# Performance work log

Hardware: AMD Instinct MI355X
Metric: run time of the kernel (lower is better)

The kernel has to match this reference:

```python
import jax, jax.numpy as jnp
import numpy as np

O, T = 2000, 6000
DIN, DW, DG, H = 2048, 300, 512, 512
VO, VR, L_EXTRA = 1000, 500, 4


def _mlp2(x, Wa, ba, Wb, bb):
    # two-layer MLP with ReLU after every Linear (sg2im build_mlp, final_nonlinearity=True)
    return jax.nn.relu(jax.nn.relu(x @ Wa + ba) @ Wb + bb)


def _triple_conv(obj_vecs, pred_vecs, s, o, Wa, ba, Wb, bb, W2a, b2a, W2b, b2b, alpha=1.0):
    # gather-by-edge -> edge MLP -> scatter-avg back to nodes (GraphTripleConv, pooling='avg')
    n_obj = obj_vecs.shape[0]
    dout = W2b.shape[1]
    cur = jnp.concatenate([obj_vecs[s], pred_vecs, obj_vecs[o]], axis=1)  # [T, 2*Din+Dp]
    t = _mlp2(cur, Wa, ba, Wb, bb)                                        # [T, 2H+Dout]
    new_s, new_p, new_o = t[:, :H], t[:, H:H + dout], t[:, H + dout:]
    pooled = jnp.zeros((n_obj, H), t.dtype).at[s].add(new_s).at[o].add(new_o)
    cnt = jnp.zeros((n_obj,), t.dtype).at[s].add(1.0).at[o].add(1.0)
    pooled = pooled / jnp.maximum(cnt, 1.0)[:, None]
    new_obj = alpha * _mlp2(pooled, W2a, b2a, W2b, b2b)
    return new_obj, new_p


def setup_inputs() -> dict:
    key = jax.random.key(0)
    ks = jax.random.split(key, 32)
    w = lambda k, sh: (jax.random.normal(k, sh, jnp.float32) * 0.02)
    inp = {
        'obj_embs': jax.random.normal(ks[0], (O, DIN), jnp.float32),
        'obj_nums': O,
        'pred_embs': jax.random.normal(ks[1], (T, DIN), jnp.float32),
        'pred_nums': T,
        'rels': jax.random.randint(ks[2], (T, 3), 0, VR, jnp.int64 if jax.config.read('jax_enable_x64') else jnp.int32),
        'objs': jax.random.randint(ks[3], (O,), 0, VO, jnp.int64 if jax.config.read('jax_enable_x64') else jnp.int32),
        # embedding tables
        'obj_table': jax.random.uniform(ks[4], (VO, DW), jnp.float32, -0.1, 0.1),
        'rel_table': jax.random.uniform(ks[5], (VR, DW), jnp.float32, -0.1, 0.1),
        # fusion layers: Linear(img_dim+word_dim -> img_dim) + relu
        'Wf_obj': w(ks[6], (DIN + DW, DIN)), 'bf_obj': jnp.zeros((DIN,), jnp.float32),
        'Wf_rel': w(ks[7], (DIN + DW, DIN)), 'bf_rel': jnp.zeros((DIN,), jnp.float32),
        # GraphTripleConv layer 1: net1 [3*DIN -> H -> 2H+DG], net2 [H -> H -> DG]
        'W1a': w(ks[8], (3 * DIN, H)), 'b1a': jnp.zeros((H,), jnp.float32),
        'W1b': w(ks[9], (H, 2 * H + DG)), 'b1b': jnp.zeros((2 * H + DG,), jnp.float32),
        'W2a': w(ks[10], (H, H)), 'b2a': jnp.zeros((H,), jnp.float32),
        'W2b': w(ks[11], (H, DG)), 'b2b': jnp.zeros((DG,), jnp.float32),
        # GraphTripleConvNet: 4 more layers, net1 [3*DG -> H -> 2H+DG], net2 [H -> H -> DG]
        'Ws1a': w(ks[12], (L_EXTRA, 3 * DG, H)), 'bs1a': jnp.zeros((L_EXTRA, H), jnp.float32),
        'Ws1b': w(ks[13], (L_EXTRA, H, 2 * H + DG)), 'bs1b': jnp.zeros((L_EXTRA, 2 * H + DG), jnp.float32),
        'Ws2a': w(ks[14], (L_EXTRA, H, H)), 'bs2a': jnp.zeros((L_EXTRA, H), jnp.float32),
        'Ws2b': w(ks[15], (L_EXTRA, H, DG)), 'bs2b': jnp.zeros((L_EXTRA, DG), jnp.float32),
    }
    return inp


def reference(obj_embs, obj_nums, pred_embs, pred_nums, rels, objs,
              obj_table, rel_table, Wf_obj, bf_obj, Wf_rel, bf_rel,
              W1a, b1a, W1b, b1b, W2a, b2a, W2b, b2b,
              Ws1a, bs1a, Ws1b, bs1b, Ws2a, bs2a, Ws2b, bs2b):
    s, p, o = rels[:, 0], rels[:, 1], rels[:, 2]
    # embedding lookup + concatenate-fusion (FusionLayer with relu)
    obj_vecs = jax.nn.relu(jnp.concatenate([obj_embs, obj_table[objs]], axis=1) @ Wf_obj + bf_obj)
    pred_vecs = jax.nn.relu(jnp.concatenate([pred_embs, rel_table[p]], axis=1) @ Wf_rel + bf_rel)
    # first GraphTripleConv (img_dim -> gconv_dim)
    obj_vecs, pred_vecs = _triple_conv(obj_vecs, pred_vecs, s, o,
                                       W1a, b1a, W1b, b1b, W2a, b2a, W2b, b2b)
    # GraphTripleConvNet: 4 more layers (gconv_dim -> gconv_dim)
    for i in range(L_EXTRA):
        obj_vecs, pred_vecs = _triple_conv(obj_vecs, pred_vecs, s, o,
                                           Ws1a[i], bs1a[i], Ws1b[i], bs1b[i],
                                           Ws2a[i], bs2a[i], Ws2b[i], bs2b[i])
    # no_imgnorm=True -> no final l2norm
    return obj_vecs, pred_vecs
```

## Files before the change

kernel.cpp:

```cpp
#include <hip/hip_runtime.h>

#define O_N 2000
#define T_N 6000
#define DIN 2048
#define DW  300
#define DG  512
#define HH_ 512

typedef __attribute__((ext_vector_type(8)))  short short8;
typedef __attribute__((ext_vector_type(16))) float f32x16;
typedef unsigned short u16;

__device__ __forceinline__ float4 ld4(const float* p) { return *(const float4*)p; }

__device__ __forceinline__ u16 rbf(float x) {
    unsigned int u = __float_as_uint(x);
    u += 0x7FFFu + ((u >> 16) & 1u);
    return (u16)(u >> 16);
}
__device__ __forceinline__ float fbf(u16 h) {
    return __uint_as_float((unsigned int)h << 16);
}
__device__ __forceinline__ void split3(float x, short& h, short& m, short& l) {
    u16 a = rbf(x);
    float r = x - fbf(a);
    u16 b = rbf(r);
    r -= fbf(b);
    u16 c = rbf(r);
    h = (short)a; m = (short)b; l = (short)c;
}

__device__ __forceinline__ void gl_lds16(u16* lds, const u16* g) {
    auto* gp = (const __attribute__((address_space(1))) unsigned int*)g;
    auto* lp = (__attribute__((address_space(3))) unsigned int*)lds;
    __builtin_amdgcn_global_load_lds(gp, lp, 16, 0, 0);
}

template<int BM, int BN, int KS>
__global__ __launch_bounds__(KS ? 512 : 256, KS ? 2 : (BM == 64 ? 4 : 2))
void gemm_mx(
    const u16* __restrict__ Ap, int MpA,
    const u16* __restrict__ Bp, int N, int KC, int M,
    const float* __restrict__ bias, int doRelu,
    float* __restrict__ C, int ldc,
    u16* __restrict__ Op, int MpO,
    const u16* __restrict__ Bp2, float* __restrict__ C2, u16* __restrict__ Op2,
    int nbx)
{
    static_assert(BM == 128 || BM == 64, "BM in {64,128}");
    constexpr int WM = BM / 2, WN = BN / 2;
    constexpr int FI = WM / 32, FJ = WN / 32;
    static_assert(!KS || FI == 2, "KS path needs FI=2");
    constexpr int UA = 6 * BM;
    constexpr int UB = 6 * BN;
    constexpr int NI = (UA + UB) / 64;
    constexpr int II = (NI + 3) / 4;
    constexpr int BUF = (BM + BN) * 48;
    __shared__ u16 sm[(KS ? 4 : 2) * BUF];

    const int tid = threadIdx.x;
    const int w = tid >> 6, lane = tid & 63;
    const int wg = w & 3;
    const int g = KS ? (w >> 2) : 0;
    const int ln31 = lane & 31, lq = lane >> 5;

    int bx = blockIdx.x;
    const u16* Bpl = Bp; float* Cl = C; u16* Opl = Op;
    if (bx >= nbx) { bx -= nbx; Bpl = Bp2; Cl = C2; Opl = Op2; }
    const int n0 = bx * BN, m0 = blockIdx.y * BM;
    const long psA = (long)KC * MpA * 8;
    const long psB = (long)KC * N * 8;

    int c0 = 0, cn = KC;
    if (KS) { int h = (KC >> 2) << 1; c0 = g ? h : 0; cn = g ? (KC - h) : h; }
    const u16* ApG = Ap + (long)c0 * MpA * 8;
    const u16* BpG = Bpl + (long)c0 * N * 8;
    u16* smg = sm + g * 2 * BUF;

    const u16* gb[II]; int gstep[II]; int lob[II]; bool gv[II];
#pragma unroll
    for (int ii = 0; ii < II; ii++) {
        int n = wg + 4 * ii;
        gv[ii] = n < NI;
        int nn = gv[ii] ? n : 0;
        int u0 = nn * 64;
        bool isA = u0 < UA;
        int uu = isA ? u0 : u0 - UA;
        int dim = isA ? BM : BN;
        int row0 = uu % dim, pq = uu / dim;
        int q = pq & 1, p = pq >> 1;
        const u16* pb = (isA ? ApG : BpG) + (long)p * (isA ? psA : psB);
        int mp = isA ? MpA : N;
        gb[ii] = pb + ((long)q * mp + (isA ? m0 : n0) + row0 + lane) * 8;
        gstep[ii] = mp * 16;
        lob[ii] = (isA ? (pq * BM + row0) : (6 * BM + pq * BN + row0)) * 8;
    }

    f32x16 ah[FI][FJ], al[FI][FJ];
#pragma unroll
    for (int fi = 0; fi < FI; fi++)
#pragma unroll
        for (int fj = 0; fj < FJ; fj++)
#pragma unroll
            for (int r = 0; r < 16; r++) { ah[fi][fj][r] = 0.f; al[fi][fj][r] = 0.f; }

    const int T = cn >> 1;
#pragma unroll
    for (int ii = 0; ii < II; ii++)
        if (gv[ii]) gl_lds16(smg + lob[ii], gb[ii]);
    __syncthreads();

    for (int t = 0; t < T; t++) {
        const int cb = (t & 1) * BUF, nb2 = ((t + 1) & 1) * BUF;
        if (t + 1 < T) {
#pragma unroll
            for (int ii = 0; ii < II; ii++)
                if (gv[ii]) gl_lds16(smg + nb2 + lob[ii],
                                     gb[ii] + (long)(t + 1) * gstep[ii]);
        }
        const u16* ab = smg + cb;
        const u16* bb = ab + 6 * BM * 8;
        short8 af[FI][3];
#pragma unroll
        for (int fi = 0; fi < FI; fi++)
#pragma unroll
            for (int p = 0; p < 3; p++)
                af[fi][p] = *(const short8*)(ab + ((p * 2 + lq) * BM + (wg >> 1) * WM + fi * 32 + ln31) * 8);
#pragma unroll
        for (int fj = 0; fj < FJ; fj++) {
            const int rB = (wg & 1) * WN + fj * 32 + ln31;
            short8 bh = *(const short8*)(bb + ((0 * 2 + lq) * BN + rB) * 8);
            short8 bm_ = *(const short8*)(bb + ((1 * 2 + lq) * BN + rB) * 8);
            short8 bl = *(const short8*)(bb + ((2 * 2 + lq) * BN + rB) * 8);
#pragma unroll
            for (int fi = 0; fi < FI; fi++) {
                ah[fi][fj] = __builtin_amdgcn_mfma_f32_32x32x16_bf16(af[fi][0], bh,  ah[fi][fj], 0, 0, 0);
                al[fi][fj] = __builtin_amdgcn_mfma_f32_32x32x16_bf16(af[fi][0], bm_, al[fi][fj], 0, 0, 0);
                al[fi][fj] = __builtin_amdgcn_mfma_f32_32x32x16_bf16(af[fi][1], bh,  al[fi][fj], 0, 0, 0);
                al[fi][fj] = __builtin_amdgcn_mfma_f32_32x32x16_bf16(af[fi][0], bl,  al[fi][fj], 0, 0, 0);
                al[fi][fj] = __builtin_amdgcn_mfma_f32_32x32x16_bf16(af[fi][1], bm_, al[fi][fj], 0, 0, 0);
                al[fi][fj] = __builtin_amdgcn_mfma_f32_32x32x16_bf16(af[fi][2], bh,  al[fi][fj], 0, 0, 0);
            }
        }
        __syncthreads();
    }

    float tv[FJ][16];
    if (KS) {
        constexpr int XW = FJ * 16 * 64;
        float* xs = (float*)sm;
        float* wrp = xs + (1 - g) * 4 * XW + wg * XW;
        if (g == 0) {
#pragma unroll
            for (int fj = 0; fj < FJ; fj++)
#pragma unroll
                for (int r = 0; r < 16; r++)
                    wrp[(fj * 16 + r) * 64 + lane] = ah[1][fj][r] + al[1][fj][r];
        } else {
#pragma unroll
            for (int fj = 0; fj < FJ; fj++)
#pragma unroll
                for (int r = 0; r < 16; r++)
                    wrp[(fj * 16 + r) * 64 + lane] = ah[0][fj][r] + al[0][fj][r];
        }
        __syncthreads();
        float* rdp = xs + g * 4 * XW + wg * XW;
        if (g == 0) {
#pragma unroll
            for (int fj = 0; fj < FJ; fj++)
#pragma unroll
                for (int r = 0; r < 16; r++)
                    tv[fj][r] = ah[0][fj][r] + al[0][fj][r] + rdp[(fj * 16 + r) * 64 + lane];
        } else {
#pragma unroll
            for (int fj = 0; fj < FJ; fj++)
#pragma unroll
                for (int r = 0; r < 16; r++)
                    tv[fj][r] = ah[1][fj][r] + al[1][fj][r] + rdp[(fj * 16 + r) * 64 + lane];
        }
        __syncthreads();
    }

    float* bounce = (float*)sm + w * 1184;
    const long psO = (long)N * MpO;
#pragma unroll
    for (int fi = 0; fi < FI; fi++) {
        if (KS && fi != g) continue;
#pragma unroll
        for (int fj = 0; fj < FJ; fj++) {
            const int colBase = n0 + (wg & 1) * WN + fj * 32;
            const int rowBase = m0 + (wg >> 1) * WM + fi * 32;
            float bv = bias ? bias[colBase + ln31] : 0.f;
            float v[16];
#pragma unroll
            for (int r = 0; r < 16; r++) {
                float s = KS ? tv[fj][r] : (ah[fi][fj][r] + al[fi][fj][r]);
                float x = s + bv;
                if (doRelu) x = fmaxf(x, 0.f);
                v[r] = x;
            }
            if (Cl) {
#pragma unroll
                for (int r = 0; r < 16; r++) {
                    int row = rowBase + (r & 3) + 8 * (r >> 2) + 4 * lq;
                    if (row < M)
                        Cl[(long)row * ldc + colBase + ln31] = v[r];
                }
            }
            if (Opl) {
#pragma unroll
                for (int r = 0; r < 16; r++)
                    bounce[((r & 3) + 8 * (r >> 2) + 4 * lq) * 36 + ln31] = v[r];
#pragma unroll
                for (int u = 0; u < 2; u++) {
                    int urow = ln31, uc = lq + 2 * u;
                    const float* rp = bounce + urow * 36 + uc * 8;
                    short8 h8, m8, l8;
#pragma unroll
                    for (int j = 0; j < 8; j++) {
                        short a, b, c2; split3(rp[j], a, b, c2);
                        h8[j] = a; m8[j] = b; l8[j] = c2;
                    }
                    long cIdx = (long)((colBase + uc * 8) >> 3);
                    long base = (cIdx * MpO + rowBase + urow) * 8;
                    *(short8*)(Opl + base) = h8;
                    *(short8*)(Opl + psO + base) = m8;
                    *(short8*)(Opl + 2 * psO + base) = l8;
                }
            }
        }
    }
}

__global__ __launch_bounds__(256) void split_b(
    const float* __restrict__ W, int K, int N, int KC,
    u16* __restrict__ Op)
{
    __shared__ float tl[64][65];
    const int tid = threadIdx.x;
    const int n0 = blockIdx.x * 64, k0 = blockIdx.y * 64;
    const long ps = (long)KC * N * 8;
#pragma unroll
    for (int l = 0; l < 4; l++) {
        int k = (tid >> 4) + l * 16;
        int nn = (tid & 15) << 2;
        float4 v = make_float4(0.f, 0.f, 0.f, 0.f);
        if (k0 + k < K) v = ld4(W + (long)(k0 + k) * N + n0 + nn);
        tl[k][nn] = v.x; tl[k][nn + 1] = v.y; tl[k][nn + 2] = v.z; tl[k][nn + 3] = v.w;
    }
    __syncthreads();
#pragma unroll
    for (int l = 0; l < 2; l++) {
        int u = tid + l * 256;
        int n = u & 63, c = u >> 6;
        short8 h8, m8, l8;
#pragma unroll
        for (int j = 0; j < 8; j++) {
            short a, b, c2; split3(tl[c * 8 + j][n], a, b, c2);
            h8[j] = a; m8[j] = b; l8[j] = c2;
        }
        long base = ((long)(k0 / 8 + c) * N + n0 + n) * 8;
        *(short8*)(Op + base) = h8;
        *(short8*)(Op + ps + base) = m8;
        *(short8*)(Op + 2 * ps + base) = l8;
    }
}

__device__ __forceinline__ void store_planes(u16* Op, long ps, long base, const float* x)
{
    short8 h8, m8, l8;
#pragma unroll
    for (int j = 0; j < 8; j++) {
        short a, b, c2; split3(x[j], a, b, c2);
        h8[j] = a; m8[j] = b; l8[j] = c2;
    }
    *(short8*)(Op + base) = h8;
    *(short8*)(Op + ps + base) = m8;
    *(short8*)(Op + 2 * ps + base) = l8;
}

__global__ __launch_bounds__(256) void split_concat_a(
    const float* __restrict__ E, int ldE, int KA,
    const float* __restrict__ Tab, int DWc,
    const int* __restrict__ idx, int idxStride,
    int mBase, int Mvalid, int Mp, int KC,
    u16* __restrict__ Op)
{
    int m = blockIdx.x * 256 + threadIdx.x;
    if (m >= Mp) return;
    int c = blockIdx.y;
    int gm = mBase + m;
    float x[8];
    if (gm >= Mvalid) {
#pragma unroll
        for (int j = 0; j < 8; j++) x[j] = 0.f;
    } else {
        int k0 = c * 8;
        if (k0 + 8 <= KA) {
            float4 a = ld4(E + (long)gm * ldE + k0);
            float4 b = ld4(E + (long)gm * ldE + k0 + 4);
            x[0] = a.x; x[1] = a.y; x[2] = a.z; x[3] = a.w;
            x[4] = b.x; x[5] = b.y; x[6] = b.z; x[7] = b.w;
        } else {
            const float* tr = Tab + (long)idx[(long)gm * idxStride] * DWc;
#pragma unroll
            for (int j = 0; j < 8; j++) {
                int k = k0 + j;
                x[j] = (k < KA) ? E[(long)gm * ldE + k]
                                : ((k - KA) < DWc ? tr[k - KA] : 0.f);
            }
        }
    }
    store_planes(Op, (long)KC * Mp * 8, ((long)c * Mp + m) * 8, x);
}

__global__ __launch_bounds__(256) void edge_planes(
    const float* __restrict__ PPv, const float* __restrict__ P1v,
    const float* __restrict__ P2v, const int* __restrict__ rels,
    const float* __restrict__ b1a, int Mp, u16* __restrict__ Op)
{
    int m = blockIdx.x * 256 + threadIdx.x;
    if (m >= Mp) return;
    int c = blockIdx.y;
    float x[8];
    if (m >= T_N) {
#pragma unroll
        for (int j = 0; j < 8; j++) x[j] = 0.f;
    } else {
        int s = rels[3 * m], o = rels[3 * m + 2];
        const float* pp = PPv + (long)m * HH_ + c * 8;
        const float* p1 = P1v + (long)s * HH_ + c * 8;
        const float* p2 = P2v + (long)o * HH_ + c * 8;
        const float* bb = b1a + c * 8;
#pragma unroll
        for (int j = 0; j < 8; j++)
            x[j] = fmaxf(pp[j] + p1[j] + p2[j] + bb[j], 0.f);
    }
    store_planes(Op, (long)64 * Mp * 8, ((long)c * Mp + m) * 8, x);
}

__global__ __launch_bounds__(256) void pool_planes(
    const float* __restrict__ PO, const int* __restrict__ CNT,
    int Mp, u16* __restrict__ Op)
{
    int m = blockIdx.x * 256 + threadIdx.x;
    if (m >= Mp) return;
    int c = blockIdx.y;
    float x[8];
    if (m >= O_N) {
#pragma unroll
        for (int j = 0; j < 8; j++) x[j] = 0.f;
    } else {
        int cc = CNT[m]; float cf = 1.f / (float)(cc < 1 ? 1 : cc);
#pragma unroll
        for (int j = 0; j < 8; j++) x[j] = PO[(long)m * HH_ + c * 8 + j] * cf;
    }
    store_planes(Op, (long)64 * Mp * 8, ((long)c * Mp + m) * 8, x);
}

__global__ __launch_bounds__(256) void predcopy_planes(
    const float* __restrict__ T2, int Mp, u16* __restrict__ Op)
{
    int m = blockIdx.x * 256 + threadIdx.x;
    if (m >= Mp) return;
    int c = blockIdx.y;
    float x[8];
    if (m >= T_N) {
#pragma unroll
        for (int j = 0; j < 8; j++) x[j] = 0.f;
    } else {
#pragma unroll
        for (int j = 0; j < 8; j++) x[j] = T2[(long)m * 1536 + 512 + c * 8 + j];
    }
    store_planes(Op, (long)64 * Mp * 8, ((long)c * Mp + m) * 8, x);
}

__global__ void predcopy_f32(const float* __restrict__ T2, float* __restrict__ dst)
{
    int i = blockIdx.x * 256 + threadIdx.x;
    if (i >= T_N * HH_ / 4) return;
    int e = i / (HH_ / 4);
    int j = (i % (HH_ / 4)) << 2;
    float4 v = ld4(T2 + (long)e * 1536 + 512 + j);
    *(float4*)(dst + (long)e * HH_ + j) = v;
}

__global__ void count_edges(const int* __restrict__ rels, int* __restrict__ CNT)
{
    int e = blockIdx.x * 256 + threadIdx.x;
    if (e >= T_N) return;
    atomicAdd(CNT + rels[3 * e + 0], 1);
    atomicAdd(CNT + rels[3 * e + 2], 1);
}

__global__ void scatter_pool(const float* __restrict__ T2,
                             const int* __restrict__ rels,
                             float* __restrict__ PO)
{
    int e = blockIdx.x;
    int t = threadIdx.x;
    int s = rels[e * 3 + 0];
    int o = rels[e * 3 + 2];
#pragma unroll
    for (int u = 0; u < 2; u++) {
        int j = t + u * 256;
        unsafeAtomicAdd(PO + (long)s * HH_ + j, T2[(long)e * 1536 + j]);
        unsafeAtomicAdd(PO + (long)o * HH_ + j, T2[(long)e * 1536 + 1024 + j]);
    }
}

template<int BM, int BN>
static inline void GX(hipStream_t st, const u16* Ap, int MpA,
                      const u16* Bp, int N, int KC, int M,
                      const float* bias, int relu_,
                      float* C, int ldc, u16* Op, int MpO,
                      const u16* Bp2, float* C2, u16* Op2)
{
    int nbx = N / BN;
    int pair = (Bp2 != nullptr) ? 2 : 1;
    dim3 g(nbx * pair, MpA / BM), b(256);
    gemm_mx<BM, BN, 0><<<g, b, 0, st>>>(Ap, MpA, Bp, N, KC, M, bias, relu_,
                                        C, ldc, Op, MpO, Bp2, C2, Op2, nbx);
}

template<int BM, int BN>
static inline void GK2(hipStream_t st, const u16* Ap, int MpA,
                       const u16* Bp, int N, int KC, int M,
                       const float* bias, int relu_,
                       float* C, int ldc, u16* Op, int MpO)
{
    dim3 g(N / BN, MpA / BM), b(512);
    gemm_mx<BM, BN, 1><<<g, b, 0, st>>>(Ap, MpA, Bp, N, KC, M, bias, relu_,
                                        C, ldc, Op, MpO,
                                        nullptr, nullptr, nullptr, N / BN);
}

static inline void SB(hipStream_t st, const float* W, int K, int N, int KC, u16* Op)
{
    dim3 g(N / 64, KC / 8), b(256);
    split_b<<<g, b, 0, st>>>(W, K, N, KC, Op);
}

extern "C" void kernel_launch(void* const* d_in, const int* in_sizes, int n_in,
                              void* d_out, int out_size, void* d_ws, size_t ws_size,
                              hipStream_t stream)
{
    const float* obj_embs  = (const float*)d_in[0];
    const float* pred_embs = (const float*)d_in[2];
    const int*   rels      = (const int*)d_in[4];
    const int*   objs      = (const int*)d_in[5];
    const float* obj_table = (const float*)d_in[6];
    const float* rel_table = (const float*)d_in[7];
    const float* Wf_obj = (const float*)d_in[8];
    const float* bf_obj = (const float*)d_in[9];
    const float* Wf_rel = (const float*)d_in[10];
    const float* bf_rel = (const float*)d_in[11];
    const float* W1a = (const float*)d_in[12];
    const float* b1a = (const float*)d_in[13];
    const float* W1b = (const float*)d_in[14];
    const float* b1b = (const float*)d_in[15];
    const float* W2a = (const float*)d_in[16];
    const float* b2a = (const float*)d_in[17];
    const float* W2b = (const float*)d_in[18];
    const float* b2b = (const float*)d_in[19];
    const float* Ws1a = (const float*)d_in[20];
    const float* bs1a = (const float*)d_in[21];
    const float* Ws1b = (const float*)d_in[22];
    const float* bs1b = (const float*)d_in[23];
    const float* Ws2a = (const float*)d_in[24];
    const float* bs2a = (const float*)d_in[25];
    const float* Ws2b = (const float*)d_in[26];
    const float* bs2b = (const float*)d_in[27];
    float* out = (float*)d_out;

    unsigned char* B8 = (unsigned char*)d_ws;
    constexpr size_t S1O  = 0;
    constexpr size_t S2O  = 29097984;
    constexpr size_t S3AO = 54263808;
    constexpr size_t ZSZ  = 86507520;
    constexpr size_t T2O  = 0;
    constexpr size_t TTO  = 36864000;
    constexpr size_t PVO  = 55345152;
    constexpr size_t PLO  = 73826304;
    constexpr size_t OVO  = 80117760;
    constexpr size_t S3BO = ZSZ;
    constexpr size_t S3CO = S3BO + 6291456;
    constexpr size_t PPO  = S3CO + 6291456;
    constexpr size_t P1O  = PPO + 12288000;
    constexpr size_t P2O  = P1O + 4096000;
    constexpr size_t CNO  = P2O + 4096000;

    u16* S1  = (u16*)(B8 + S1O);
    u16* S2  = (u16*)(B8 + S2O);
    u16* S3A = (u16*)(B8 + S3AO);
    u16* S3B = (u16*)(B8 + S3BO);
    u16* S3C = (u16*)(B8 + S3CO);
    float* T2 = (float*)(B8 + T2O);
    u16* TTp  = (u16*)(B8 + TTO);
    u16* Hp   = (u16*)(B8 + TTO);
    u16* PVp  = (u16*)(B8 + PVO);
    u16* PLp  = (u16*)(B8 + PLO);
    u16* OVp  = (u16*)(B8 + OVO);
    float* PP = (float*)(B8 + PPO);
    float* P1 = (float*)(B8 + P1O);
    float* P2 = (float*)(B8 + P2O);
    float* PO = P1;
    int* CNT  = (int*)(B8 + CNO);

    hipMemsetAsync(CNT, 0, O_N * sizeof(int), stream);
    hipLaunchKernelGGL(count_edges, dim3((T_N + 255) / 256), dim3(256), 0, stream, rels, CNT);

    SB(stream, Wf_obj, DIN + DW, DIN, 296, S3A);
    {
        dim3 g(8, 296), b(256);
        split_concat_a<<<g, b, 0, stream>>>(obj_embs, DIN, DIN, obj_table, DW,
                                            objs, 1, 0, O_N, 2048, 296, S1);
    }
    GK2<128, 128>(stream, S1, 2048, S3A, DIN, 296, O_N, bf_obj, 1,
                  nullptr, 0, S2, 2048);
    SB(stream, W1a, DIN, HH_, 256, S3B);
    SB(stream, W1a + (size_t)2 * DIN * HH_, DIN, HH_, 256, S3C);
    GX<64, 64>(stream, S2, 2048, S3B, HH_, 256, O_N, nullptr, 0,
               P1, HH_, nullptr, 0, S3C, P2, nullptr);
    SB(stream, Wf_rel, DIN + DW, DIN, 296, S3A);
    SB(stream, W1a + (size_t)DIN * HH_, DIN, HH_, 256, S3B);
    for (int ch = 0; ch < 3; ch++) {
        int ch0 = ch * 2048;
        int mp  = (ch == 2) ? 1920 : 2048;
        int mv  = (ch == 2) ? 1904 : 2048;
        dim3 g((mp + 255) / 256, 296), b(256);
        split_concat_a<<<g, b, 0, stream>>>(pred_embs, DIN, DIN, rel_table, DW,
                                            rels + 1, 3, ch0, T_N, mp, 296, S1);
        GK2<128, 128>(stream, S1, mp, S3A, DIN, 296, mv, bf_rel, 1,
                      nullptr, 0, S2, mp);
        GX<64, 64>(stream, S2, mp, S3B, HH_, 256, mv, nullptr, 0,
                   PP + (size_t)ch0 * HH_, HH_, nullptr, 0,
                   nullptr, nullptr, nullptr);
    }

    for (int L = 0; L < 5; L++) {
        const float* bb1a = (L == 0) ? b1a : (bs1a + (size_t)(L - 1) * HH_);
        const float* w1b  = (L == 0) ? W1b : (Ws1b + (size_t)(L - 1) * HH_ * 1536);
        const float* bb1b = (L == 0) ? b1b : (bs1b + (size_t)(L - 1) * 1536);
        const float* w2a  = (L == 0) ? W2a : (Ws2a + (size_t)(L - 1) * HH_ * HH_);
        const float* bb2a = (L == 0) ? b2a : (bs2a + (size_t)(L - 1) * HH_);
        const float* w2b  = (L == 0) ? W2b : (Ws2b + (size_t)(L - 1) * HH_ * DG);
        const float* bb2b = (L == 0) ? b2b : (bs2b + (size_t)(L - 1) * DG);

        if (L > 0) {
            const float* w1a = Ws1a + (size_t)(L - 1) * 3 * HH_ * HH_;
            SB(stream, w1a, HH_, HH_, 64, S3B);
            SB(stream, w1a + (size_t)2 * HH_ * HH_, HH_, HH_, 64, S3C);
            GX<64, 64>(stream, OVp, 2048, S3B, HH_, 64, O_N, nullptr, 0,
                       P1, HH_, nullptr, 0, S3C, P2, nullptr);
            SB(stream, w1a + (size_t)HH_ * HH_, HH_, HH_, 64, S3B);
            GX<64, 64>(stream, PVp, 6016, S3B, HH_, 64, T_N, nullptr, 0,
                       PP, HH_, nullptr, 0, nullptr, nullptr, nullptr);
        }

        {
            dim3 g(24, 64), b(256);
            edge_planes<<<g, b, 0, stream>>>(PP, P1, P2, rels, bb1a, 6016, TTp);
        }
        SB(stream, w1b, HH_, 1536, 64, S3C);
        GX<128, 128>(stream, TTp, 6016, S3C, 1536, 64, T_N, bb1b, 1,
                     T2, 1536, nullptr, 0, nullptr, nullptr, nullptr);
        hipMemsetAsync(PO, 0, (size_t)O_N * HH_ * sizeof(float), stream);
        hipLaunchKernelGGL(scatter_pool, dim3(T_N), dim3(256), 0, stream, T2, rels, PO);
        {
            dim3 g(8, 64), b(256);
            pool_planes<<<g, b, 0, stream>>>(PO, CNT, 2048, PLp);
        }
        SB(stream, w2a, HH_, HH_, 64, S3B);
        GX<64, 64>(stream, PLp, 2048, S3B, HH_, 64, O_N, bb2a, 1,
                   nullptr, 0, Hp, 2048, nullptr, nullptr, nullptr);
        SB(stream, w2b, HH_, DG, 64, S3C);
        if (L < 4) {
            GX<64, 64>(stream, Hp, 2048, S3C, DG, 64, O_N, bb2b, 1,
                       nullptr, 0, OVp, 2048, nullptr, nullptr, nullptr);
            dim3 g(24, 64), b(256);
            predcopy_planes<<<g, b, 0, stream>>>(T2, 6016, PVp);
        } else {
            GX<64, 64>(stream, Hp, 2048, S3C, DG, 64, O_N, bb2b, 1,
                       out, DG, nullptr, 0, nullptr, nullptr, nullptr);
            hipLaunchKernelGGL(predcopy_f32, dim3((T_N * HH_ / 4 + 255) / 256),
                               dim3(256), 0, stream, T2, out + (size_t)O_N * DG);
        }
    }
}
```

Measured before the change: 2.011 ms.

## Triple-buffer GEMM LDS tiles with prefetch depth two and explicit vmcnt waits

Moves the split-bf16 MFMA GEMM main loop from double to triple buffering in LDS, issuing global-to-LDS loads two k-steps ahead. Explicit s_waitcnt vmcnt counts with raw s_barrier replace __syncthreads, so only the oldest stage's loads are awaited. All fragments are read from LDS before a second barrier and the MFMAs run afterwards, which lets the buffer be refilled while compute proceeds. The cost is 1.5x LDS per block, which may lower occupancy. The hand-computed vmcnt values rely on every wave issuing exactly LDMIN loads per stage, which could break if the per-wave load count differs.

```diff
diff --git a/kernel.cpp b/kernel.cpp
--- a/kernel.cpp
+++ b/kernel.cpp
@@ -55,8 +55,9 @@
     constexpr int UB = 6 * BN;
     constexpr int NI = (UA + UB) / 64;
     constexpr int II = (NI + 3) / 4;
+    constexpr int LDMIN = NI / 4;
     constexpr int BUF = (BM + BN) * 48;
-    __shared__ u16 sm[(KS ? 4 : 2) * BUF];
+    __shared__ u16 sm[(KS ? 6 : 3) * BUF];
 
     const int tid = threadIdx.x;
     const int w = tid >> 6, lane = tid & 63;
@@ -75,7 +76,7 @@
     if (KS) { int h = (KC >> 2) << 1; c0 = g ? h : 0; cn = g ? (KC - h) : h; }
     const u16* ApG = Ap + (long)c0 * MpA * 8;
     const u16* BpG = Bpl + (long)c0 * N * 8;
-    u16* smg = sm + g * 2 * BUF;
+    u16* smg = sm + g * 3 * BUF;
 
     const u16* gb[II]; int gstep[II]; int lob[II]; bool gv[II];
 #pragma unroll
@@ -107,20 +108,33 @@
     const int T = cn >> 1;
 #pragma unroll
     for (int ii = 0; ii < II; ii++)
-        if (gv[ii]) gl_lds16(smg + lob[ii], gb[ii]);
-    __syncthreads();
-
+        if (gv[ii]) { gl_lds16(smg + lob[ii], gb[ii]); }
+    if (T > 1) {
+#pragma unroll
+        for (int ii = 0; ii < II; ii++)
+            if (gv[ii]) gl_lds16(smg + BUF + lob[ii], gb[ii] + (long)gstep[ii]);
+    }
+#pragma unroll
+    for (int ii = 0; ii < II; ii++) gb[ii] += (long)2 * gstep[ii];
+
+    int cb = 0, sb = 2 * BUF;
     for (int t = 0; t < T; t++) {
-        const int cb = (t & 1) * BUF, nb2 = ((t + 1) & 1) * BUF;
-        if (t + 1 < T) {
+        if (t + 2 < T) {
 #pragma unroll
             for (int ii = 0; ii < II; ii++)
-                if (gv[ii]) gl_lds16(smg + nb2 + lob[ii],
-                                     gb[ii] + (long)(t + 1) * gstep[ii]);
-        }
+                if (gv[ii]) gl_lds16(smg + sb + lob[ii], gb[ii]);
+#pragma unroll
+            for (int ii = 0; ii < II; ii++) gb[ii] += (long)gstep[ii];
+        }
+        if (t + 2 < T)      asm volatile("s_waitcnt vmcnt(%0)" :: "i"(2 * LDMIN) : "memory");
+        else if (t + 1 < T) asm volatile("s_waitcnt vmcnt(%0)" :: "i"(LDMIN) : "memory");
+        else                asm volatile("s_waitcnt vmcnt(0)" ::: "memory");
+        __builtin_amdgcn_s_barrier();
+        asm volatile("" ::: "memory");
+
         const u16* ab = smg + cb;
         const u16* bb = ab + 6 * BM * 8;
-        short8 af[FI][3];
+        short8 af[FI][3], bf[FJ][3];
 #pragma unroll
         for (int fi = 0; fi < FI; fi++)
 #pragma unroll
@@ -129,20 +143,28 @@
 #pragma unroll
         for (int fj = 0; fj < FJ; fj++) {
             const int rB = (wg & 1) * WN + fj * 32 + ln31;
-            short8 bh = *(const short8*)(bb + ((0 * 2 + lq) * BN + rB) * 8);
-            short8 bm_ = *(const short8*)(bb + ((1 * 2 + lq) * BN + rB) * 8);
-            short8 bl = *(const short8*)(bb + ((2 * 2 + lq) * BN + rB) * 8);
+#pragma unroll
+            for (int p = 0; p < 3; p++)
+                bf[fj][p] = *(const short8*)(bb + ((p * 2 + lq) * BN + rB) * 8);
+        }
+        asm volatile("s_waitcnt lgkmcnt(0)" ::: "memory");
+        __builtin_amdgcn_s_barrier();
+        asm volatile("" ::: "memory");
+
+#pragma unroll
+        for (int fj = 0; fj < FJ; fj++) {
 #pragma unroll
             for (int fi = 0; fi < FI; fi++) {
-                ah[fi][fj] = __builtin_amdgcn_mfma_f32_32x32x16_bf16(af[fi][0], bh,  ah[fi][fj], 0, 0, 0);
-                al[fi][fj] = __builtin_amdgcn_mfma_f32_32x32x16_bf16(af[fi][0], bm_, al[fi][fj], 0, 0, 0);
-                al[fi][fj] = __builtin_amdgcn_mfma_f32_32x32x16_bf16(af[fi][1], bh,  al[fi][fj], 0, 0, 0);
-                al[fi][fj] = __builtin_amdgcn_mfma_f32_32x32x16_bf16(af[fi][0], bl,  al[fi][fj], 0, 0, 0);
-                al[fi][fj] = __builtin_amdgcn_mfma_f32_32x32x16_bf16(af[fi][1], bm_, al[fi][fj], 0, 0, 0);
-                al[fi][fj] = __builtin_amdgcn_mfma_f32_32x32x16_bf16(af[fi][2], bh,  al[fi][fj], 0, 0, 0);
+                ah[fi][fj] = __builtin_amdgcn_mfma_f32_32x32x16_bf16(af[fi][0], bf[fj][0], ah[fi][fj], 0, 0, 0);
+                al[fi][fj] = __builtin_amdgcn_mfma_f32_32x32x16_bf16(af[fi][0], bf[fj][1], al[fi][fj], 0, 0, 0);
+                al[fi][fj] = __builtin_amdgcn_mfma_f32_32x32x16_bf16(af[fi][1], bf[fj][0], al[fi][fj], 0, 0, 0);
+                al[fi][fj] = __builtin_amdgcn_mfma_f32_32x32x16_bf16(af[fi][0], bf[fj][2], al[fi][fj], 0, 0, 0);
+                al[fi][fj] = __builtin_amdgcn_mfma_f32_32x32x16_bf16(af[fi][1], bf[fj][1], al[fi][fj], 0, 0, 0);
+                al[fi][fj] = __builtin_amdgcn_mfma_f32_32x32x16_bf16(af[fi][2], bf[fj][0], al[fi][fj], 0, 0, 0);
             }
         }
-        __syncthreads();
+        cb += BUF; if (cb == 3 * BUF) cb = 0;
+        sb += BUF; if (sb == 3 * BUF) sb = 0;
     }
 
     float tv[FJ][16];
```

New measurement: 1.772 ms. 11.9% less time.
